# Kernel tuning notes

Hardware: AMD Instinct MI355X
Metric: run time of the kernel (lower is better)

The kernel has to match this reference:

```python
import jax, jax.numpy as jnp
import numpy as np

N_NODES = 50000
N_EDGES = 800000
D = 128


def _gcn_conv(x, edge_index, W, b):
    """PyG GCNConv: out = D^{-1/2} (A + I) D^{-1/2} (x W) + b.

    edge_index[0] = source nodes, edge_index[1] = target nodes.
    Self-loops handled analytically instead of materializing them.
    """
    n = x.shape[0]
    src, dst = edge_index[0], edge_index[1]
    h = x @ W  # [N, out]
    # degree with self-loop: in-degree of target + 1
    deg = jax.ops.segment_sum(jnp.ones_like(dst, dtype=h.dtype), dst, num_segments=n) + 1.0
    dinv = jax.lax.rsqrt(deg)  # deg >= 1, safe
    norm = dinv[src] * dinv[dst]  # [E]
    msgs = norm[:, None] * h[src]  # [E, out]  (the big irregular-gather intermediate)
    agg = jax.ops.segment_sum(msgs, dst, num_segments=n)
    # self-loop contribution: norm = dinv[i]*dinv[i] = 1/deg
    agg = agg + h * (1.0 / deg)[:, None]
    return agg + b


def setup_inputs() -> dict:
    key = jax.random.key(0)
    k1, k2, k3, k4 = jax.random.split(key, 4)
    x = jax.random.normal(k1, (N_NODES, D), dtype=jnp.float32)
    edge_index = jax.random.randint(k2, (2, N_EDGES), 0, N_NODES, dtype=jnp.int64)
    scale = 1.0 / np.sqrt(D)
    W1 = jax.random.normal(k3, (D, D), dtype=jnp.float32) * scale
    W2 = jax.random.normal(k4, (D, D), dtype=jnp.float32) * scale
    b1 = jnp.zeros((D,), dtype=jnp.float32)
    b2 = jnp.zeros((D,), dtype=jnp.float32)
    return {"x": x, "edge_index": edge_index, "W1": W1, "b1": b1, "W2": W2, "b2": b2}


def reference(x, edge_index, W1, b1, W2, b2):
    h = _gcn_conv(x, edge_index, W1, b1)
    h = jax.nn.relu(h)  # dropout p=0.0 -> identity
    out = _gcn_conv(h, edge_index, W2, b2)
    return out
```

## Files before the change

kernel.cpp:

```cpp
#include <hip/hip_runtime.h>

#define DF 128
#define NBKT_MAX 256
#define CAP 8192
#define SCHUNK 2048

typedef unsigned int uint;
typedef unsigned short ushort;
typedef __attribute__((ext_vector_type(8))) short short8;
typedef __attribute__((ext_vector_type(4))) float f32x4;

union frag_u { uint4 u4; short8 s8; };

__device__ __forceinline__ uint f2u(float f) { return __float_as_uint(f); }
__device__ __forceinline__ ushort rne_bf16(float v) {
    uint u = __float_as_uint(v);
    u = u + 0x7FFFu + ((u >> 16) & 1u);
    return (ushort)(u >> 16);
}
__device__ __forceinline__ float bflo(uint u) { return __uint_as_float(u << 16); }
__device__ __forceinline__ float bfhi(uint u) { return __uint_as_float(u & 0xFFFF0000u); }

__global__ __launch_bounds__(256) void scatter_wprep(const int* __restrict__ src,
                                                     const int* __restrict__ dst,
                                                     int* __restrict__ ccur,
                                                     uint* __restrict__ ebuf,
                                                     int E, int NB, int SB,
                                                     const float* __restrict__ W1,
                                                     const float* __restrict__ W2,
                                                     uint4* __restrict__ Whi,
                                                     uint4* __restrict__ Wlo) {
    __shared__ int cnt[NBKT_MAX];
    __shared__ int base[NBKT_MAX];
    int t = threadIdx.x;
    if ((int)blockIdx.x < SB) {
        int e0 = blockIdx.x * SCHUNK;
        int eb0 = e0 + t * 8;
        int lim = min(E - eb0, 8);
        int d[8], s[8];
        if (lim == 8) {
            int4 d0 = *(const int4*)(dst + eb0), d1 = *(const int4*)(dst + eb0 + 4);
            int4 s0 = *(const int4*)(src + eb0), s1 = *(const int4*)(src + eb0 + 4);
            d[0] = d0.x; d[1] = d0.y; d[2] = d0.z; d[3] = d0.w;
            d[4] = d1.x; d[5] = d1.y; d[6] = d1.z; d[7] = d1.w;
            s[0] = s0.x; s[1] = s0.y; s[2] = s0.z; s[3] = s0.w;
            s[4] = s1.x; s[5] = s1.y; s[6] = s1.z; s[7] = s1.w;
        } else {
            for (int i = 0; i < 8; ++i) { d[i] = 0; s[i] = 0; }
            for (int i = 0; i < lim; ++i) { d[i] = dst[eb0 + i]; s[i] = src[eb0 + i]; }
        }
        for (int i = t; i < NB; i += 256) cnt[i] = 0;
        __syncthreads();
        for (int i = 0; i < 8; ++i)
            if (i < lim) atomicAdd(&cnt[d[i] >> 8], 1);
        __syncthreads();
        for (int i = t; i < NB; i += 256) base[i] = cnt[i] ? atomicAdd(&ccur[i], cnt[i]) : 0;
        __syncthreads();
        for (int i = 0; i < 8; ++i)
            if (i < lim) {
                int b = d[i] >> 8;
                int pos = atomicAdd(&base[b], 1);
                if (pos < CAP) ebuf[(size_t)b * CAP + pos] = ((uint)(d[i] & 255) << 24) | (uint)s[i];
            }
    } else {
        int tt4 = ((int)blockIdx.x - SB) * 256 + t;
        int wsel = tt4 >> 11;
        int tt = tt4 & 2047;
        const float* W = wsel ? W2 : W1;
        int lane = tt & 63;
        int n  = ((tt >> 6) & 7) * 16 + (lane & 15);
        int k0 = (tt >> 9) * 32 + (lane >> 4) * 8;
        uint hi[4], lo[4];
#pragma unroll
        for (int p = 0; p < 4; ++p) {
            float f0 = W[(size_t)(k0 + 2 * p) * DF + n];
            float f1 = W[(size_t)(k0 + 2 * p + 1) * DF + n];
            uint u0 = f2u(f0), u1 = f2u(f1);
            hi[p] = (u1 & 0xFFFF0000u) | (u0 >> 16);
            float l0 = f0 - __uint_as_float(u0 & 0xFFFF0000u);
            float l1 = f1 - __uint_as_float(u1 & 0xFFFF0000u);
            lo[p] = (f2u(l1) & 0xFFFF0000u) | (f2u(l0) >> 16);
        }
        Whi[wsel * 2048 + tt] = make_uint4(hi[0], hi[1], hi[2], hi[3]);
        Wlo[wsel * 2048 + tt] = make_uint4(lo[0], lo[1], lo[2], lo[3]);
    }
}

__global__ __launch_bounds__(256) void sort_gemm1(const uint* __restrict__ ebuf,
                                                  const int* __restrict__ ccur,
                                                  int* __restrict__ rstart,
                                                  int* __restrict__ rend,
                                                  float* __restrict__ dinv,
                                                  ushort* __restrict__ srcs,
                                                  const float* __restrict__ A,
                                                  const uint4* __restrict__ Bhi,
                                                  const uint4* __restrict__ Blo,
                                                  ushort* __restrict__ Hq,
                                                  int NB, int N) {
    __shared__ int cnt[256];
    __shared__ int sp[256];
    int t = threadIdx.x;
    if ((int)blockIdx.x < NB) {
        int b = blockIdx.x;
        int count = min(ccur[b], CAP);
        const uint* eb = ebuf + (size_t)b * CAP;
        if (b == 0) {
            if (t < 16) {
                size_t byteoff = ((size_t)(t >> 2) * (N + 1) + N) * 64 + (size_t)(t & 3) * 16;
                *(uint4*)((char*)Hq + byteoff) = make_uint4(0u, 0u, 0u, 0u);
            } else if (t == 16) {
                dinv[N] = 0.0f;
            }
        }
        cnt[t] = 0;
        __syncthreads();
        for (int j = t; j < count; j += 256) atomicAdd(&cnt[eb[j] >> 24], 1);
        __syncthreads();
        int v = cnt[t];
        int pv = (v + 7) & ~7;
        sp[t] = pv;
        __syncthreads();
        for (int off = 1; off < 256; off <<= 1) {
            int x = (t >= off) ? sp[t - off] : 0;
            __syncthreads();
            sp[t] += x;
            __syncthreads();
        }
        int ex = sp[t] - pv;
        int node = b * 256 + t;
        if (node < N) {
            rstart[node] = b * CAP + ex;
            rend[node]   = b * CAP + ex + v;
            dinv[node] = rsqrtf((float)v + 1.0f);
        }
        for (int p = ex + v; p < ex + pv && p < CAP; ++p)
            srcs[(size_t)b * CAP + p] = (ushort)N;
        sp[t] = ex;
        __syncthreads();
        for (int j = t; j < count; j += 256) {
            uint e = eb[j];
            int pos = atomicAdd(&sp[e >> 24], 1);
            if (pos < CAP) srcs[(size_t)b * CAP + pos] = (ushort)(e & 0xFFFFFFu);
        }
    } else {
        const int lane = t & 63;
        const int w = t >> 6;
        const int l15 = lane & 15, quad = lane >> 4;
        const int rowbase = ((int)blockIdx.x - NB) * 128 + w * 32;
        const int M = N;

        f32x4 acc[2][8];
#pragma unroll
        for (int rt = 0; rt < 2; ++rt)
#pragma unroll
            for (int ct = 0; ct < 8; ++ct) acc[rt][ct] = (f32x4){0.f, 0.f, 0.f, 0.f};

        for (int q = 0; q < 4; ++q) {
            frag_u ah[2], al[2];
#pragma unroll
            for (int rt = 0; rt < 2; ++rt) {
                int m = rowbase + rt * 16 + l15;
                if (m >= M) m = M - 1;
                const float* ap = A + (size_t)m * DF + q * 32 + quad * 8;
                float4 v0 = *(const float4*)ap;
                float4 v1 = *(const float4*)(ap + 4);
                float f[8] = {v0.x, v0.y, v0.z, v0.w, v1.x, v1.y, v1.z, v1.w};
                uint hi[4], lo[4];
#pragma unroll
                for (int p = 0; p < 4; ++p) {
                    uint u0 = f2u(f[2 * p]), u1 = f2u(f[2 * p + 1]);
                    hi[p] = (u1 & 0xFFFF0000u) | (u0 >> 16);
                    float l0 = f[2 * p]     - __uint_as_float(u0 & 0xFFFF0000u);
                    float l1 = f[2 * p + 1] - __uint_as_float(u1 & 0xFFFF0000u);
                    lo[p] = (f2u(l1) & 0xFFFF0000u) | (f2u(l0) >> 16);
                }
                ah[rt].u4 = make_uint4(hi[0], hi[1], hi[2], hi[3]);
                al[rt].u4 = make_uint4(lo[0], lo[1], lo[2], lo[3]);
            }
#pragma unroll
            for (int ct = 0; ct < 8; ++ct) {
                frag_u bh, bl;
                bh.u4 = Bhi[(q * 8 + ct) * 64 + lane];
                bl.u4 = Blo[(q * 8 + ct) * 64 + lane];
#pragma unroll
                for (int rt = 0; rt < 2; ++rt) {
                    acc[rt][ct] = __builtin_amdgcn_mfma_f32_16x16x32_bf16(al[rt].s8, bh.s8, acc[rt][ct], 0, 0, 0);
                    acc[rt][ct] = __builtin_amdgcn_mfma_f32_16x16x32_bf16(ah[rt].s8, bl.s8, acc[rt][ct], 0, 0, 0);
                    acc[rt][ct] = __builtin_amdgcn_mfma_f32_16x16x32_bf16(ah[rt].s8, bh.s8, acc[rt][ct], 0, 0, 0);
                }
            }
        }
#pragma unroll
        for (int rt = 0; rt < 2; ++rt)
#pragma unroll
            for (int reg = 0; reg < 4; ++reg) {
                int row = rowbase + rt * 16 + quad * 4 + reg;
                if (row < M) {
#pragma unroll
                    for (int ct = 0; ct < 8; ++ct)
                        Hq[((size_t)(ct >> 1) * (M + 1) + row) * 32 + (ct & 1) * 16 + l15] =
                            rne_bf16(acc[rt][ct][reg]);
                }
            }
    }
}

__global__ __launch_bounds__(256) void gemm_bf16A(const ushort* __restrict__ A,
                                                  const uint4* __restrict__ Bhi,
                                                  const uint4* __restrict__ Blo,
                                                  const float* __restrict__ dinv,
                                                  ushort* __restrict__ Hq, int M) {
    const int lane = threadIdx.x & 63;
    const int w = threadIdx.x >> 6;
    const int l15 = lane & 15, quad = lane >> 4;
    const int rowbase = blockIdx.x * 128 + w * 32;

    f32x4 acc[2][8];
#pragma unroll
    for (int rt = 0; rt < 2; ++rt)
#pragma unroll
        for (int ct = 0; ct < 8; ++ct) acc[rt][ct] = (f32x4){0.f, 0.f, 0.f, 0.f};

    for (int q = 0; q < 4; ++q) {
        frag_u a[2];
#pragma unroll
        for (int rt = 0; rt < 2; ++rt) {
            int m = rowbase + rt * 16 + l15;
            if (m >= M) m = M - 1;
            const ushort* ap = A + ((size_t)q * M + m) * 32 + quad * 8;
            a[rt].u4 = *(const uint4*)ap;
        }
#pragma unroll
        for (int ct = 0; ct < 8; ++ct) {
            frag_u bh, bl;
            bh.u4 = Bhi[(q * 8 + ct) * 64 + lane];
            bl.u4 = Blo[(q * 8 + ct) * 64 + lane];
#pragma unroll
            for (int rt = 0; rt < 2; ++rt) {
                acc[rt][ct] = __builtin_amdgcn_mfma_f32_16x16x32_bf16(a[rt].s8, bl.s8, acc[rt][ct], 0, 0, 0);
                acc[rt][ct] = __builtin_amdgcn_mfma_f32_16x16x32_bf16(a[rt].s8, bh.s8, acc[rt][ct], 0, 0, 0);
            }
        }
    }
#pragma unroll
    for (int rt = 0; rt < 2; ++rt)
#pragma unroll
        for (int reg = 0; reg < 4; ++reg) {
            int row = rowbase + rt * 16 + quad * 4 + reg;
            if (row < M) {
                float di = dinv[row];
#pragma unroll
                for (int ct = 0; ct < 8; ++ct)
                    Hq[((size_t)(ct >> 1) * (M + 1) + row) * 32 + (ct & 1) * 16 + l15] =
                        rne_bf16(acc[rt][ct][reg] * di);
            }
        }
}

template<bool L1>
__global__ __launch_bounds__(256) void quarter_gather(const uint4* __restrict__ H4,
                                                      const float* __restrict__ dinv,
                                                      const int* __restrict__ rstart,
                                                      const int* __restrict__ rend,
                                                      const ushort* __restrict__ srcs,
                                                      const float* __restrict__ bias,
                                                      void* __restrict__ outv, int N) {
    int t = threadIdx.x;
    int bid = blockIdx.x;
    int sub = bid & 7;
    int q = sub >> 1;
    int n = (bid >> 3) * 128 + (sub & 1) * 64 + (t >> 2);
    if (n >= N) return;
    int l = t & 3;
    const uint4* Hq4 = H4 + (size_t)q * (N + 1) * 4;

    float4 bb0 = ((const float4*)bias)[q * 8 + l * 2];
    float4 bb1 = ((const float4*)bias)[q * 8 + l * 2 + 1];

    float di = dinv[n];
    uint4 self = Hq4[(size_t)n * 4 + l];
    float sc = L1 ? di : 1.0f;
    float a0 = bflo(self.x) * sc, a1 = bfhi(self.x) * sc, a2 = bflo(self.y) * sc, a3 = bfhi(self.y) * sc;
    float a4 = bflo(self.z) * sc, a5 = bfhi(self.z) * sc, a6 = bflo(self.w) * sc, a7 = bfhi(self.w) * sc;

    int j = rstart[n];
    int niter = (rend[n] - j + 7) >> 3;
    uint4 sv;
    if (niter > 0) sv = *(const uint4*)(srcs + j);
    for (int g = 0; g < niter; ++g) {
        uint4 svc = sv;
        if (g + 1 < niter) sv = *(const uint4*)(srcs + j + 8);
        int si[8];
        si[0] = svc.x & 0xFFFF; si[1] = svc.x >> 16;
        si[2] = svc.y & 0xFFFF; si[3] = svc.y >> 16;
        si[4] = svc.z & 0xFFFF; si[5] = svc.z >> 16;
        si[6] = svc.w & 0xFFFF; si[7] = svc.w >> 16;
        uint4 v[8];
#pragma unroll
        for (int i = 0; i < 8; ++i) v[i] = Hq4[(size_t)si[i] * 4 + l];
        if constexpr (L1) {
            float dd[8];
#pragma unroll
            for (int i = 0; i < 8; ++i) dd[i] = dinv[si[i]];
#pragma unroll
            for (int i = 0; i < 8; ++i) {
                a0 = fmaf(bflo(v[i].x), dd[i], a0); a1 = fmaf(bfhi(v[i].x), dd[i], a1);
                a2 = fmaf(bflo(v[i].y), dd[i], a2); a3 = fmaf(bfhi(v[i].y), dd[i], a3);
                a4 = fmaf(bflo(v[i].z), dd[i], a4); a5 = fmaf(bfhi(v[i].z), dd[i], a5);
                a6 = fmaf(bflo(v[i].w), dd[i], a6); a7 = fmaf(bfhi(v[i].w), dd[i], a7);
            }
        } else {
#pragma unroll
            for (int i = 0; i < 8; ++i) {
                a0 += bflo(v[i].x); a1 += bfhi(v[i].x);
                a2 += bflo(v[i].y); a3 += bfhi(v[i].y);
                a4 += bflo(v[i].z); a5 += bfhi(v[i].z);
                a6 += bflo(v[i].w); a7 += bfhi(v[i].w);
            }
        }
        j += 8;
    }
    float o0 = fmaf(a0, di, bb0.x), o1 = fmaf(a1, di, bb0.y);
    float o2 = fmaf(a2, di, bb0.z), o3 = fmaf(a3, di, bb0.w);
    float o4 = fmaf(a4, di, bb1.x), o5 = fmaf(a5, di, bb1.y);
    float o6 = fmaf(a6, di, bb1.z), o7 = fmaf(a7, di, bb1.w);
    if (L1) {
        o0 = fmaxf(o0, 0.f); o1 = fmaxf(o1, 0.f); o2 = fmaxf(o2, 0.f); o3 = fmaxf(o3, 0.f);
        o4 = fmaxf(o4, 0.f); o5 = fmaxf(o5, 0.f); o6 = fmaxf(o6, 0.f); o7 = fmaxf(o7, 0.f);
        uint4 pk;
        pk.x = (uint)rne_bf16(o0) | ((uint)rne_bf16(o1) << 16);
        pk.y = (uint)rne_bf16(o2) | ((uint)rne_bf16(o3) << 16);
        pk.z = (uint)rne_bf16(o4) | ((uint)rne_bf16(o5) << 16);
        pk.w = (uint)rne_bf16(o6) | ((uint)rne_bf16(o7) << 16);
        ((uint4*)outv)[((size_t)q * N + n) * 4 + l] = pk;
    } else {
        float4* op = (float4*)((float*)outv + (size_t)n * DF + q * 32 + l * 8);
        op[0] = make_float4(o0, o1, o2, o3);
        op[1] = make_float4(o4, o5, o6, o7);
    }
}

extern "C" void kernel_launch(void* const* d_in, const int* in_sizes, int n_in,
                              void* d_out, int out_size, void* d_ws, size_t ws_size,
                              hipStream_t stream) {
    const float* x  = (const float*)d_in[0];
    const int*   ei = (const int*)d_in[1];
    const float* W1 = (const float*)d_in[2];
    const float* b1 = (const float*)d_in[3];
    const float* W2 = (const float*)d_in[4];
    const float* b2 = (const float*)d_in[5];

    const int N = in_sizes[0] / DF;
    const int E = in_sizes[1] / 2;
    const int* src = ei;
    const int* dstp = ei + E;
    const int NB = (N + 255) >> 8;
    const int SB = (E + SCHUNK - 1) / SCHUNK;

    float* out = (float*)d_out;
    char* ws = (char*)d_ws;
    size_t off = 0;
    auto carve = [&](size_t bytes) { void* p = ws + off; off += (bytes + 255) & ~(size_t)255; return p; };
    ushort* Hq     = (ushort*)carve((size_t)4 * (N + 1) * 32 * sizeof(ushort) * 2);
    ushort* Z1     = (ushort*)carve((size_t)N * DF * sizeof(ushort));
    float*  dinv   = (float*)carve((size_t)(N + 1) * sizeof(float));
    int*    rstart = (int*)carve((size_t)N * sizeof(int));
    int*    rend   = (int*)carve((size_t)N * sizeof(int));
    uint*   ebuf   = (uint*)carve((size_t)NB * CAP * sizeof(uint));
    ushort* srcs   = (ushort*)carve((size_t)NB * CAP * sizeof(ushort));
    int*    ccur   = (int*)carve(NBKT_MAX * sizeof(int));
    uint4*  Whi    = (uint4*)carve(2 * 2048 * sizeof(uint4));
    uint4*  Wlo    = (uint4*)carve(2 * 2048 * sizeof(uint4));

    const int gemm_b = (N + 127) / 128;
    const int gath_b = ((N + 127) / 128) * 8;

    hipMemsetAsync(ccur, 0, NBKT_MAX * sizeof(int), stream);
    scatter_wprep<<<SB + 16, 256, 0, stream>>>(src, dstp, ccur, ebuf, E, NB, SB, W1, W2, Whi, Wlo);

    sort_gemm1<<<NB + gemm_b, 256, 0, stream>>>(ebuf, ccur, rstart, rend, dinv, srcs,
                                                x, Whi, Wlo, Hq, NB, N);

    quarter_gather<true><<<gath_b, 256, 0, stream>>>((const uint4*)Hq, dinv, rstart, rend,
                                                     srcs, b1, Z1, N);

    gemm_bf16A<<<gemm_b, 256, 0, stream>>>(Z1, Whi + 2048, Wlo + 2048, dinv, Hq, N);
    quarter_gather<false><<<gath_b, 256, 0, stream>>>((const uint4*)Hq, dinv, rstart, rend,
                                                      srcs, b2, out, N);
}
```

Before: 189.5 us.

## Regroup kernels: co-schedule GEMM1 with edge scatter, replace memset with init kernel

Moves the weight hi/lo split and the buffer initialisation (bucket counters, padding row of Hq, dinv[N]) into a small new kernel that replaces the hipMemsetAsync call. The first feature GEMM now runs in the same launch as the edge bucket scatter instead of alongside the per-bucket sort, and the sort becomes its own kernel. The aim is to overlap the compute-heavy GEMM with the atomic-bound scatter and to drop the memset. The cost is an extra kernel launch and a different grouping of blocks within each launch.

```diff
diff --git a/kernel.cpp b/kernel.cpp
--- a/kernel.cpp
+++ b/kernel.cpp
@@ -21,15 +21,121 @@
 __device__ __forceinline__ float bflo(uint u) { return __uint_as_float(u << 16); }
 __device__ __forceinline__ float bfhi(uint u) { return __uint_as_float(u & 0xFFFF0000u); }
 
-__global__ __launch_bounds__(256) void scatter_wprep(const int* __restrict__ src,
+__global__ __launch_bounds__(256) void wsplit_init(const float* __restrict__ W1,
+                                                   const float* __restrict__ W2,
+                                                   uint4* __restrict__ Whi,
+                                                   uint4* __restrict__ Wlo,
+                                                   int* __restrict__ ccur,
+                                                   ushort* __restrict__ Hq,
+                                                   float* __restrict__ dinv,
+                                                   int N) {
+    int t = threadIdx.x;
+    int tt4 = (int)blockIdx.x * 256 + t;
+    int wsel = tt4 >> 11;
+    int tt = tt4 & 2047;
+    const float* W = wsel ? W2 : W1;
+    int lane = tt & 63;
+    int n  = ((tt >> 6) & 7) * 16 + (lane & 15);
+    int k0 = (tt >> 9) * 32 + (lane >> 4) * 8;
+    uint hi[4], lo[4];
+#pragma unroll
+    for (int p = 0; p < 4; ++p) {
+        float f0 = W[(size_t)(k0 + 2 * p) * DF + n];
+        float f1 = W[(size_t)(k0 + 2 * p + 1) * DF + n];
+        uint u0 = f2u(f0), u1 = f2u(f1);
+        hi[p] = (u1 & 0xFFFF0000u) | (u0 >> 16);
+        float l0 = f0 - __uint_as_float(u0 & 0xFFFF0000u);
+        float l1 = f1 - __uint_as_float(u1 & 0xFFFF0000u);
+        lo[p] = (f2u(l1) & 0xFFFF0000u) | (f2u(l0) >> 16);
+    }
+    Whi[wsel * 2048 + tt] = make_uint4(hi[0], hi[1], hi[2], hi[3]);
+    Wlo[wsel * 2048 + tt] = make_uint4(lo[0], lo[1], lo[2], lo[3]);
+    if (blockIdx.x == 0) {
+        ccur[t] = 0;
+    } else if (blockIdx.x == 1) {
+        if (t < 16) {
+            size_t byteoff = ((size_t)(t >> 2) * (N + 1) + N) * 64 + (size_t)(t & 3) * 16;
+            *(uint4*)((char*)Hq + byteoff) = make_uint4(0u, 0u, 0u, 0u);
+        } else if (t == 16) {
+            dinv[N] = 0.0f;
+        }
+    }
+}
+
+__device__ __forceinline__ void gemm1_body(int gb, int t,
+                                           const float* __restrict__ A,
+                                           const uint4* __restrict__ Bhi,
+                                           const uint4* __restrict__ Blo,
+                                           ushort* __restrict__ Hq, int M) {
+    const int lane = t & 63;
+    const int w = t >> 6;
+    const int l15 = lane & 15, quad = lane >> 4;
+    const int rowbase = gb * 128 + w * 32;
+
+    f32x4 acc[2][8];
+#pragma unroll
+    for (int rt = 0; rt < 2; ++rt)
+#pragma unroll
+        for (int ct = 0; ct < 8; ++ct) acc[rt][ct] = (f32x4){0.f, 0.f, 0.f, 0.f};
+
+    for (int q = 0; q < 4; ++q) {
+        frag_u ah[2], al[2];
+#pragma unroll
+        for (int rt = 0; rt < 2; ++rt) {
+            int m = rowbase + rt * 16 + l15;
+            if (m >= M) m = M - 1;
+            const float* ap = A + (size_t)m * DF + q * 32 + quad * 8;
+            float4 v0 = *(const float4*)ap;
+            float4 v1 = *(const float4*)(ap + 4);
+            float f[8] = {v0.x, v0.y, v0.z, v0.w, v1.x, v1.y, v1.z, v1.w};
+            uint hi[4], lo[4];
+#pragma unroll
+            for (int p = 0; p < 4; ++p) {
+                uint u0 = f2u(f[2 * p]), u1 = f2u(f[2 * p + 1]);
+                hi[p] = (u1 & 0xFFFF0000u) | (u0 >> 16);
+                float l0 = f[2 * p]     - __uint_as_float(u0 & 0xFFFF0000u);
+                float l1 = f[2 * p + 1] - __uint_as_float(u1 & 0xFFFF0000u);
+                lo[p] = (f2u(l1) & 0xFFFF0000u) | (f2u(l0) >> 16);
+            }
+            ah[rt].u4 = make_uint4(hi[0], hi[1], hi[2], hi[3]);
+            al[rt].u4 = make_uint4(lo[0], lo[1], lo[2], lo[3]);
+        }
+#pragma unroll
+        for (int ct = 0; ct < 8; ++ct) {
+            frag_u bh, bl;
+            bh.u4 = Bhi[(q * 8 + ct) * 64 + lane];
+            bl.u4 = Blo[(q * 8 + ct) * 64 + lane];
+#pragma unroll
+            for (int rt = 0; rt < 2; ++rt) {
+                acc[rt][ct] = __builtin_amdgcn_mfma_f32_16x16x32_bf16(al[rt].s8, bh.s8, acc[rt][ct], 0, 0, 0);
+                acc[rt][ct] = __builtin_amdgcn_mfma_f32_16x16x32_bf16(ah[rt].s8, bl.s8, acc[rt][ct], 0, 0, 0);
+                acc[rt][ct] = __builtin_amdgcn_mfma_f32_16x16x32_bf16(ah[rt].s8, bh.s8, acc[rt][ct], 0, 0, 0);
+            }
+        }
+    }
+#pragma unroll
+    for (int rt = 0; rt < 2; ++rt)
+#pragma unroll
+        for (int reg = 0; reg < 4; ++reg) {
+            int row = rowbase + rt * 16 + quad * 4 + reg;
+            if (row < M) {
+#pragma unroll
+                for (int ct = 0; ct < 8; ++ct)
+                    Hq[((size_t)(ct >> 1) * (M + 1) + row) * 32 + (ct & 1) * 16 + l15] =
+                        rne_bf16(acc[rt][ct][reg]);
+            }
+        }
+}
+
+__global__ __launch_bounds__(256) void scatter_gemm1(const int* __restrict__ src,
                                                      const int* __restrict__ dst,
                                                      int* __restrict__ ccur,
                                                      uint* __restrict__ ebuf,
                                                      int E, int NB, int SB,
-                                                     const float* __restrict__ W1,
-                                                     const float* __restrict__ W2,
-                                                     uint4* __restrict__ Whi,
-                                                     uint4* __restrict__ Wlo) {
+                                                     const float* __restrict__ A,
+                                                     const uint4* __restrict__ Bhi,
+                                                     const uint4* __restrict__ Blo,
+                                                     ushort* __restrict__ Hq, int N) {
     __shared__ int cnt[NBKT_MAX];
     __shared__ int base[NBKT_MAX];
     int t = threadIdx.x;
@@ -63,145 +169,51 @@
                 if (pos < CAP) ebuf[(size_t)b * CAP + pos] = ((uint)(d[i] & 255) << 24) | (uint)s[i];
             }
     } else {
-        int tt4 = ((int)blockIdx.x - SB) * 256 + t;
-        int wsel = tt4 >> 11;
-        int tt = tt4 & 2047;
-        const float* W = wsel ? W2 : W1;
-        int lane = tt & 63;
-        int n  = ((tt >> 6) & 7) * 16 + (lane & 15);
-        int k0 = (tt >> 9) * 32 + (lane >> 4) * 8;
-        uint hi[4], lo[4];
-#pragma unroll
-        for (int p = 0; p < 4; ++p) {
-            float f0 = W[(size_t)(k0 + 2 * p) * DF + n];
-            float f1 = W[(size_t)(k0 + 2 * p + 1) * DF + n];
-            uint u0 = f2u(f0), u1 = f2u(f1);
-            hi[p] = (u1 & 0xFFFF0000u) | (u0 >> 16);
-            float l0 = f0 - __uint_as_float(u0 & 0xFFFF0000u);
-            float l1 = f1 - __uint_as_float(u1 & 0xFFFF0000u);
-            lo[p] = (f2u(l1) & 0xFFFF0000u) | (f2u(l0) >> 16);
-        }
-        Whi[wsel * 2048 + tt] = make_uint4(hi[0], hi[1], hi[2], hi[3]);
-        Wlo[wsel * 2048 + tt] = make_uint4(lo[0], lo[1], lo[2], lo[3]);
-    }
-}
-
-__global__ __launch_bounds__(256) void sort_gemm1(const uint* __restrict__ ebuf,
-                                                  const int* __restrict__ ccur,
-                                                  int* __restrict__ rstart,
-                                                  int* __restrict__ rend,
-                                                  float* __restrict__ dinv,
-                                                  ushort* __restrict__ srcs,
-                                                  const float* __restrict__ A,
-                                                  const uint4* __restrict__ Bhi,
-                                                  const uint4* __restrict__ Blo,
-                                                  ushort* __restrict__ Hq,
-                                                  int NB, int N) {
+        gemm1_body((int)blockIdx.x - SB, t, A, Bhi, Blo, Hq, N);
+    }
+}
+
+__global__ __launch_bounds__(256) void sort_only(const uint* __restrict__ ebuf,
+                                                 const int* __restrict__ ccur,
+                                                 int* __restrict__ rstart,
+                                                 int* __restrict__ rend,
+                                                 float* __restrict__ dinv,
+                                                 ushort* __restrict__ srcs,
+                                                 int N) {
     __shared__ int cnt[256];
     __shared__ int sp[256];
-    int t = threadIdx.x;
-    if ((int)blockIdx.x < NB) {
-        int b = blockIdx.x;
-        int count = min(ccur[b], CAP);
-        const uint* eb = ebuf + (size_t)b * CAP;
-        if (b == 0) {
-            if (t < 16) {
-                size_t byteoff = ((size_t)(t >> 2) * (N + 1) + N) * 64 + (size_t)(t & 3) * 16;
-                *(uint4*)((char*)Hq + byteoff) = make_uint4(0u, 0u, 0u, 0u);
-            } else if (t == 16) {
-                dinv[N] = 0.0f;
-            }
-        }
-        cnt[t] = 0;
+    int t = threadIdx.x, b = blockIdx.x;
+    int count = min(ccur[b], CAP);
+    const uint* eb = ebuf + (size_t)b * CAP;
+    cnt[t] = 0;
+    __syncthreads();
+    for (int j = t; j < count; j += 256) atomicAdd(&cnt[eb[j] >> 24], 1);
+    __syncthreads();
+    int v = cnt[t];
+    int pv = (v + 7) & ~7;
+    sp[t] = pv;
+    __syncthreads();
+    for (int off = 1; off < 256; off <<= 1) {
+        int x = (t >= off) ? sp[t - off] : 0;
         __syncthreads();
-        for (int j = t; j < count; j += 256) atomicAdd(&cnt[eb[j] >> 24], 1);
+        sp[t] += x;
         __syncthreads();
-        int v = cnt[t];
-        int pv = (v + 7) & ~7;
-        sp[t] = pv;
-        __syncthreads();
-        for (int off = 1; off < 256; off <<= 1) {
-            int x = (t >= off) ? sp[t - off] : 0;
-            __syncthreads();
-            sp[t] += x;
-            __syncthreads();
-        }
-        int ex = sp[t] - pv;
-        int node = b * 256 + t;
-        if (node < N) {
-            rstart[node] = b * CAP + ex;
-            rend[node]   = b * CAP + ex + v;
-            dinv[node] = rsqrtf((float)v + 1.0f);
-        }
-        for (int p = ex + v; p < ex + pv && p < CAP; ++p)
-            srcs[(size_t)b * CAP + p] = (ushort)N;
-        sp[t] = ex;
-        __syncthreads();
-        for (int j = t; j < count; j += 256) {
-            uint e = eb[j];
-            int pos = atomicAdd(&sp[e >> 24], 1);
-            if (pos < CAP) srcs[(size_t)b * CAP + pos] = (ushort)(e & 0xFFFFFFu);
-        }
-    } else {
-        const int lane = t & 63;
-        const int w = t >> 6;
-        const int l15 = lane & 15, quad = lane >> 4;
-        const int rowbase = ((int)blockIdx.x - NB) * 128 + w * 32;
-        const int M = N;
-
-        f32x4 acc[2][8];
-#pragma unroll
-        for (int rt = 0; rt < 2; ++rt)
-#pragma unroll
-            for (int ct = 0; ct < 8; ++ct) acc[rt][ct] = (f32x4){0.f, 0.f, 0.f, 0.f};
-
-        for (int q = 0; q < 4; ++q) {
-            frag_u ah[2], al[2];
-#pragma unroll
-            for (int rt = 0; rt < 2; ++rt) {
-                int m = rowbase + rt * 16 + l15;
-                if (m >= M) m = M - 1;
-                const float* ap = A + (size_t)m * DF + q * 32 + quad * 8;
-                float4 v0 = *(const float4*)ap;
-                float4 v1 = *(const float4*)(ap + 4);
-                float f[8] = {v0.x, v0.y, v0.z, v0.w, v1.x, v1.y, v1.z, v1.w};
-                uint hi[4], lo[4];
-#pragma unroll
-                for (int p = 0; p < 4; ++p) {
-                    uint u0 = f2u(f[2 * p]), u1 = f2u(f[2 * p + 1]);
-                    hi[p] = (u1 & 0xFFFF0000u) | (u0 >> 16);
-                    float l0 = f[2 * p]     - __uint_as_float(u0 & 0xFFFF0000u);
-                    float l1 = f[2 * p + 1] - __uint_as_float(u1 & 0xFFFF0000u);
-                    lo[p] = (f2u(l1) & 0xFFFF0000u) | (f2u(l0) >> 16);
-                }
-                ah[rt].u4 = make_uint4(hi[0], hi[1], hi[2], hi[3]);
-                al[rt].u4 = make_uint4(lo[0], lo[1], lo[2], lo[3]);
-            }
-#pragma unroll
-            for (int ct = 0; ct < 8; ++ct) {
-                frag_u bh, bl;
-                bh.u4 = Bhi[(q * 8 + ct) * 64 + lane];
-                bl.u4 = Blo[(q * 8 + ct) * 64 + lane];
-#pragma unroll
-                for (int rt = 0; rt < 2; ++rt) {
-                    acc[rt][ct] = __builtin_amdgcn_mfma_f32_16x16x32_bf16(al[rt].s8, bh.s8, acc[rt][ct], 0, 0, 0);
-                    acc[rt][ct] = __builtin_amdgcn_mfma_f32_16x16x32_bf16(ah[rt].s8, bl.s8, acc[rt][ct], 0, 0, 0);
-                    acc[rt][ct] = __builtin_amdgcn_mfma_f32_16x16x32_bf16(ah[rt].s8, bh.s8, acc[rt][ct], 0, 0, 0);
-                }
-            }
-        }
-#pragma unroll
-        for (int rt = 0; rt < 2; ++rt)
-#pragma unroll
-            for (int reg = 0; reg < 4; ++reg) {
-                int row = rowbase + rt * 16 + quad * 4 + reg;
-                if (row < M) {
-#pragma unroll
-                    for (int ct = 0; ct < 8; ++ct)
-                        Hq[((size_t)(ct >> 1) * (M + 1) + row) * 32 + (ct & 1) * 16 + l15] =
-                            rne_bf16(acc[rt][ct][reg]);
-                }
-            }
+    }
+    int ex = sp[t] - pv;
+    int node = b * 256 + t;
+    if (node < N) {
+        rstart[node] = b * CAP + ex;
+        rend[node]   = b * CAP + ex + v;
+        dinv[node] = rsqrtf((float)v + 1.0f);
+    }
+    for (int p = ex + v; p < ex + pv && p < CAP; ++p)
+        srcs[(size_t)b * CAP + p] = (ushort)N;
+    sp[t] = ex;
+    __syncthreads();
+    for (int j = t; j < count; j += 256) {
+        uint e = eb[j];
+        int pos = atomicAdd(&sp[e >> 24], 1);
+        if (pos < CAP) srcs[(size_t)b * CAP + pos] = (ushort)(e & 0xFFFFFFu);
     }
 }
 
@@ -375,16 +387,18 @@
     const int gemm_b = (N + 127) / 128;
     const int gath_b = ((N + 127) / 128) * 8;
 
-    hipMemsetAsync(ccur, 0, NBKT_MAX * sizeof(int), stream);
-    scatter_wprep<<<SB + 16, 256, 0, stream>>>(src, dstp, ccur, ebuf, E, NB, SB, W1, W2, Whi, Wlo);
-
-    sort_gemm1<<<NB + gemm_b, 256, 0, stream>>>(ebuf, ccur, rstart, rend, dinv, srcs,
-                                                x, Whi, Wlo, Hq, NB, N);
+    wsplit_init<<<16, 256, 0, stream>>>(W1, W2, Whi, Wlo, ccur, Hq, dinv, N);
+
+    scatter_gemm1<<<SB + gemm_b, 256, 0, stream>>>(src, dstp, ccur, ebuf, E, NB, SB,
+                                                   x, Whi, Wlo, Hq, N);
+
+    sort_only<<<NB, 256, 0, stream>>>(ebuf, ccur, rstart, rend, dinv, srcs, N);
 
     quarter_gather<true><<<gath_b, 256, 0, stream>>>((const uint4*)Hq, dinv, rstart, rend,
                                                      srcs, b1, Z1, N);
 
     gemm_bf16A<<<gemm_b, 256, 0, stream>>>(Z1, Whi + 2048, Wlo + 2048, dinv, Hq, N);
+
     quarter_gather<false><<<gath_b, 256, 0, stream>>>((const uint4*)Hq, dinv, rstart, rend,
                                                       srcs, b2, out, N);
 }
```

Result: slower. 197.7 us (+4.3%).

## Overlap second-layer GEMM with layer-1 gather by splitting node range in halves

Applied to the files above, without the earlier changes.

Splits the layer-1 gather into two halves. The GEMM for the first half of layer 2 runs in the same launch as the gather for the second half, and the remaining GEMM blocks run after. A separate Hq2 buffer is added so the layer-2 GEMM output does not overwrite Hq while the layer-1 gather still reads it. The aim is to fill idle GPU time between the gather and GEMM phases, at the cost of one extra launch and more workspace.

```diff
diff --git a/kernel.cpp b/kernel.cpp
--- a/kernel.cpp
+++ b/kernel.cpp
@@ -96,6 +96,7 @@
                                                   const uint4* __restrict__ Bhi,
                                                   const uint4* __restrict__ Blo,
                                                   ushort* __restrict__ Hq,
+                                                  ushort* __restrict__ Hq2,
                                                   int NB, int N) {
     __shared__ int cnt[256];
     __shared__ int sp[256];
@@ -108,7 +109,11 @@
             if (t < 16) {
                 size_t byteoff = ((size_t)(t >> 2) * (N + 1) + N) * 64 + (size_t)(t & 3) * 16;
                 *(uint4*)((char*)Hq + byteoff) = make_uint4(0u, 0u, 0u, 0u);
-            } else if (t == 16) {
+            } else if (t < 32) {
+                int tz = t - 16;
+                size_t byteoff = ((size_t)(tz >> 2) * (N + 1) + N) * 64 + (size_t)(tz & 3) * 16;
+                *(uint4*)((char*)Hq2 + byteoff) = make_uint4(0u, 0u, 0u, 0u);
+            } else if (t == 32) {
                 dinv[N] = 0.0f;
             }
         }
@@ -205,15 +210,16 @@
     }
 }
 
-__global__ __launch_bounds__(256) void gemm_bf16A(const ushort* __restrict__ A,
-                                                  const uint4* __restrict__ Bhi,
-                                                  const uint4* __restrict__ Blo,
-                                                  const float* __restrict__ dinv,
-                                                  ushort* __restrict__ Hq, int M) {
-    const int lane = threadIdx.x & 63;
-    const int w = threadIdx.x >> 6;
+__device__ __forceinline__ void gemm2_body(int gb, int t,
+                                           const ushort* A,
+                                           const uint4* __restrict__ Bhi,
+                                           const uint4* __restrict__ Blo,
+                                           const float* __restrict__ dinv,
+                                           ushort* Hq, int M) {
+    const int lane = t & 63;
+    const int w = t >> 6;
     const int l15 = lane & 15, quad = lane >> 4;
-    const int rowbase = blockIdx.x * 128 + w * 32;
+    const int rowbase = gb * 128 + w * 32;
 
     f32x4 acc[2][8];
 #pragma unroll
@@ -257,19 +263,25 @@
         }
 }
 
+__global__ __launch_bounds__(256) void gemm_bf16A(const ushort* __restrict__ A,
+                                                  const uint4* __restrict__ Bhi,
+                                                  const uint4* __restrict__ Blo,
+                                                  const float* __restrict__ dinv,
+                                                  ushort* __restrict__ Hq, int M, int gb0) {
+    gemm2_body((int)blockIdx.x + gb0, threadIdx.x, A, Bhi, Blo, dinv, Hq, M);
+}
+
 template<bool L1>
-__global__ __launch_bounds__(256) void quarter_gather(const uint4* __restrict__ H4,
-                                                      const float* __restrict__ dinv,
-                                                      const int* __restrict__ rstart,
-                                                      const int* __restrict__ rend,
-                                                      const ushort* __restrict__ srcs,
-                                                      const float* __restrict__ bias,
-                                                      void* __restrict__ outv, int N) {
-    int t = threadIdx.x;
-    int bid = blockIdx.x;
-    int sub = bid & 7;
+__device__ __forceinline__ void gather_body(int chunk, int sub, int t,
+                                            const uint4* H4,
+                                            const float* __restrict__ dinv,
+                                            const int* __restrict__ rstart,
+                                            const int* __restrict__ rend,
+                                            const ushort* __restrict__ srcs,
+                                            const float* __restrict__ bias,
+                                            void* outv, int N) {
     int q = sub >> 1;
-    int n = (bid >> 3) * 128 + (sub & 1) * 64 + (t >> 2);
+    int n = chunk * 128 + (sub & 1) * 64 + (t >> 2);
     if (n >= N) return;
     int l = t & 3;
     const uint4* Hq4 = H4 + (size_t)q * (N + 1) * 4;
@@ -340,6 +352,39 @@
     }
 }
 
+template<bool L1>
+__global__ __launch_bounds__(256) void quarter_gather(const uint4* __restrict__ H4,
+                                                      const float* __restrict__ dinv,
+                                                      const int* __restrict__ rstart,
+                                                      const int* __restrict__ rend,
+                                                      const ushort* __restrict__ srcs,
+                                                      const float* __restrict__ bias,
+                                                      void* __restrict__ outv, int N,
+                                                      int chunk0) {
+    gather_body<L1>(((int)blockIdx.x >> 3) + chunk0, (int)blockIdx.x & 7, threadIdx.x,
+                    H4, dinv, rstart, rend, srcs, bias, outv, N);
+}
+
+__global__ __launch_bounds__(256) void gather1_gemm2(const uint4* H4,
+                                                     const float* __restrict__ dinv,
+                                                     const int* __restrict__ rstart,
+                                                     const int* __restrict__ rend,
+                                                     const ushort* __restrict__ srcs,
+                                                     const float* __restrict__ b1,
+                                                     ushort* Z1,
+                                                     const uint4* __restrict__ Bhi2,
+                                                     const uint4* __restrict__ Blo2,
+                                                     ushort* Hq2,
+                                                     int C1, int G2A, int N) {
+    if ((int)blockIdx.x < G2A) {
+        gemm2_body((int)blockIdx.x, threadIdx.x, (const ushort*)Z1, Bhi2, Blo2, dinv, Hq2, N);
+    } else {
+        int b = (int)blockIdx.x - G2A;
+        gather_body<true>((b >> 3) + C1, b & 7, threadIdx.x,
+                          H4, dinv, rstart, rend, srcs, b1, (void*)Z1, N);
+    }
+}
+
 extern "C" void kernel_launch(void* const* d_in, const int* in_sizes, int n_in,
                               void* d_out, int out_size, void* d_ws, size_t ws_size,
                               hipStream_t stream) {
@@ -361,7 +406,8 @@
     char* ws = (char*)d_ws;
     size_t off = 0;
     auto carve = [&](size_t bytes) { void* p = ws + off; off += (bytes + 255) & ~(size_t)255; return p; };
-    ushort* Hq     = (ushort*)carve((size_t)4 * (N + 1) * 32 * sizeof(ushort) * 2);
+    ushort* Hq     = (ushort*)carve((size_t)4 * (N + 1) * 32 * sizeof(ushort));
+    ushort* Hq2    = (ushort*)carve((size_t)4 * (N + 1) * 32 * sizeof(ushort));
     ushort* Z1     = (ushort*)carve((size_t)N * DF * sizeof(ushort));
     float*  dinv   = (float*)carve((size_t)(N + 1) * sizeof(float));
     int*    rstart = (int*)carve((size_t)N * sizeof(int));
@@ -372,19 +418,24 @@
     uint4*  Whi    = (uint4*)carve(2 * 2048 * sizeof(uint4));
     uint4*  Wlo    = (uint4*)carve(2 * 2048 * sizeof(uint4));
 
-    const int gemm_b = (N + 127) / 128;
-    const int gath_b = ((N + 127) / 128) * 8;
+    const int TC = (N + 127) / 128;
+    const int C1 = (TC + 1) / 2;
 
     hipMemsetAsync(ccur, 0, NBKT_MAX * sizeof(int), stream);
     scatter_wprep<<<SB + 16, 256, 0, stream>>>(src, dstp, ccur, ebuf, E, NB, SB, W1, W2, Whi, Wlo);
 
-    sort_gemm1<<<NB + gemm_b, 256, 0, stream>>>(ebuf, ccur, rstart, rend, dinv, srcs,
-                                                x, Whi, Wlo, Hq, NB, N);
-
-    quarter_gather<true><<<gath_b, 256, 0, stream>>>((const uint4*)Hq, dinv, rstart, rend,
-                                                     srcs, b1, Z1, N);
-
-    gemm_bf16A<<<gemm_b, 256, 0, stream>>>(Z1, Whi + 2048, Wlo + 2048, dinv, Hq, N);
-    quarter_gather<false><<<gath_b, 256, 0, stream>>>((const uint4*)Hq, dinv, rstart, rend,
-                                                      srcs, b2, out, N);
-}
+    sort_gemm1<<<NB + TC, 256, 0, stream>>>(ebuf, ccur, rstart, rend, dinv, srcs,
+                                            x, Whi, Wlo, Hq, Hq2, NB, N);
+
+    quarter_gather<true><<<C1 * 8, 256, 0, stream>>>((const uint4*)Hq, dinv, rstart, rend,
+                                                     srcs, b1, Z1, N, 0);
+
+    gather1_gemm2<<<C1 + (TC - C1) * 8, 256, 0, stream>>>((const uint4*)Hq, dinv, rstart, rend,
+                                                          srcs, b1, Z1, Whi + 2048, Wlo + 2048,
+                                                          Hq2, C1, C1, N);
+
+    gemm_bf16A<<<TC - C1, 256, 0, stream>>>(Z1, Whi + 2048, Wlo + 2048, dinv, Hq2, N, C1);
+
+    quarter_gather<false><<<TC * 8, 256, 0, stream>>>((const uint4*)Hq2, dinv, rstart, rend,
+                                                      srcs, b2, out, N, 0);
+}
```

After: 199.0 us. 5.0% more time.
